# Kernel optimization log

Measured on AMD Instinct MI355X. Metric: run time of the kernel, lower is better.

Reference implementation:

```python
import jax, jax.numpy as jnp
import numpy as np

B, N, D = 4, 1024, 1024
T_ITER = 4
E_TYPES = 4  # edge_type_num; module loops over E_TYPES+1 with bitmask
ALPHA = 0.2


def _lin_w(key, out_f, in_f):
    # fan-avg uniform init from custom Linear
    bound = float(np.sqrt(3.0 / ((in_f + out_f) / 2.0)))
    return jax.random.uniform(key, (out_f, in_f), minval=-bound, maxval=bound, dtype=jnp.float32)


def setup_inputs() -> dict:
    key = jax.random.key(0)
    ks = jax.random.split(key, 32)
    inp = {}
    inp['ents'] = jax.random.normal(ks[0], (B, N, D), jnp.float32)
    inp['ent_mask'] = jnp.ones((B, N), jnp.float32)
    inp['q_encoding'] = jax.random.normal(ks[1], (B, D), jnp.float32)
    inp['adj'] = jax.random.randint(ks[2], (B, N, N), 0, E_TYPES + 1, dtype=jnp.int32)
    inp['types'] = 30  # bits 1..4 set -> edge types 1..4 active
    inp['init_mem'] = jax.random.normal(ks[3], (1, D), jnp.float32)
    inp['w_qin'] = _lin_w(ks[4], D, D); inp['b_qin'] = jnp.zeros((D,), jnp.float32)
    inp['w_qt'] = jnp.stack([_lin_w(ks[5 + t], D, D) for t in range(T_ITER)])
    inp['b_qt'] = jnp.zeros((T_ITER, D), jnp.float32)
    inp['w_pl'] = _lin_w(ks[9], D, D);  inp['b_pl'] = jnp.zeros((D,), jnp.float32)
    inp['w_pc'] = _lin_w(ks[10], D, D); inp['b_pc'] = jnp.zeros((D,), jnp.float32)
    inp['w_q'] = _lin_w(ks[11], D, 3 * D); inp['b_q'] = jnp.zeros((D,), jnp.float32)
    inp['w_k'] = _lin_w(ks[12], D, 3 * D); inp['b_k'] = jnp.zeros((D,), jnp.float32)
    inp['w_v'] = _lin_w(ks[13], D, 3 * D); inp['b_v'] = jnp.zeros((D,), jnp.float32)
    inp['w_pk'] = _lin_w(ks[14], D, D); inp['b_pk'] = jnp.zeros((D,), jnp.float32)
    inp['w_pv'] = _lin_w(ks[15], D, D); inp['b_pv'] = jnp.zeros((D,), jnp.float32)
    # wes: xavier_uniform(gain=1.414) on shape (2D, 1); stored flat as (E_TYPES, 2D)
    wb = 1.414 * float(np.sqrt(6.0 / (2 * D + 1)))
    inp['wes'] = jax.random.uniform(ks[16], (E_TYPES, 2 * D), minval=-wb, maxval=wb, dtype=jnp.float32)
    inp['w_mu'] = _lin_w(ks[17], D, 2 * D); inp['b_mu'] = jnp.zeros((D,), jnp.float32)
    inp['w_cb'] = _lin_w(ks[18], D, 2 * D); inp['b_cb'] = jnp.zeros((D,), jnp.float32)
    return inp


def _lin(x, w, b):
    return x @ w.T + b


def _qdgat_forward(ents, ent_mask, q_encoding, adj, types, init_mem,
                   w_qin, b_qin, w_qt, b_qt, w_pl, b_pl, w_pc, b_pc,
                   w_q, b_q, w_k, b_k, w_v, b_v, w_pk, b_pk, w_pv, b_pv,
                   wes, w_mu, b_mu, w_cb, b_cb):
    d = ents.shape[-1]
    x_loc = ents
    x_ctx = jnp.broadcast_to(init_mem, ents.shape)
    # eval mode: var-drop mask is ones scaled by ent_mask
    var_drop = ent_mask[:, :, None]
    adj_pos = adj > 0
    q_base = jax.nn.elu(_lin(q_encoding, w_qin, b_qin))
    n_types = wes.shape[0] + 1  # self.edge_type_num = edge_type_num + 1
    for t in range(T_ITER):
        cmd = _lin(q_base, w_qt[t], b_qt[t])                      # [B,D]
        xc = x_ctx * var_drop
        pl = _lin(x_loc, w_pl, b_pl)
        pc = _lin(xc, w_pc, b_pc)
        x_joint = jnp.concatenate([x_loc, xc, pl * pc], axis=-1)   # [B,N,3D]
        q = _lin(x_joint, w_q, b_q)                               # [B,N,D]
        k = _lin(x_joint, w_k, b_k) * _lin(cmd, w_pk, b_pk)[:, None, :]
        v = _lin(x_joint, w_v, b_v) * _lin(cmd, w_pv, b_pv)[:, None, :]
        # edge_score[b,i,j] = sum over active types T of (adj==T) * (q_i . we[:D] + k_j . we[D:])
        # equivalent to matmul((cat(q_i,k_j) * (adj==T)), we) without materializing [B,N,N,2D]
        edge_score = jnp.zeros(adj.shape, jnp.float32)
        for i in range(n_types):
            if (types >> i) & 1 == 1:
                w1, w2 = wes[i - 1, :d], wes[i - 1, d:]  # i=0 aliases wes[-1], as in torch
                s = (q @ w1)[:, :, None] + (k @ w2)[:, None, :]    # [B,N,N]
                edge_score = edge_score + jnp.where(adj == i, s, 0.0)
        e = jnp.where(edge_score > 0, edge_score, ALPHA * edge_score)  # leaky relu
        logits = jnp.where(adj_pos, e, jnp.float32(-9e15))
        prob = jax.nn.softmax(logits, axis=-1)                     # [B,N,N]
        message = jnp.einsum('bij,bjd->bid', prob, v)
        x_ctx = _lin(jnp.concatenate([xc, message], axis=-1), w_mu, b_mu)
    return _lin(jnp.concatenate([x_loc, x_ctx], axis=-1), w_cb, b_cb)


def reference(ents, ent_mask, q_encoding, adj, types, init_mem,
              w_qin, b_qin, w_qt, b_qt, w_pl, b_pl, w_pc, b_pc,
              w_q, b_q, w_k, b_k, w_v, b_v, w_pk, b_pk, w_pv, b_pv,
              wes, w_mu, b_mu, w_cb, b_cb):
    return _qdgat_forward(ents, ent_mask, q_encoding, adj, types, init_mem,
                          w_qin, b_qin, w_qt, b_qt, w_pl, b_pl, w_pc, b_pc,
                          w_q, b_q, w_k, b_k, w_v, b_v, w_pk, b_pk, w_pv, b_pv,
                          wes, w_mu, b_mu, w_cb, b_cb)
```

## Files before the change

### kernel.cpp

```cpp
#include <hip/hip_runtime.h>
#include <hip/hip_bf16.h>
#include <stdint.h>
#include <stddef.h>


typedef __hip_bfloat16 bf16;
typedef __attribute__((ext_vector_type(8))) short short8;
typedef __attribute__((ext_vector_type(4))) float floatx4;

#define NB 4
#define NN 1024
#define DD 1024
#define NT_ITER 4
#define MM (NB * NN)

static __device__ __forceinline__ float b2f(bf16 x) { return __bfloat162float(x); }
static __device__ __forceinline__ bf16 f2b(float x) { return __float2bfloat16(x); }
static __device__ __forceinline__ unsigned short f2bu(float x) {
    bf16 h = __float2bfloat16(x);
    unsigned short u;
    __builtin_memcpy(&u, &h, 2);
    return u;
}
static __device__ __forceinline__ float bu2f(unsigned short u) {
    unsigned int t = (unsigned int)u << 16;
    float f;
    __builtin_memcpy(&f, &t, 4);
    return f;
}

static __device__ __forceinline__ void gl_lds16(const void* g, void* l) {
    __builtin_amdgcn_global_load_lds(
        (const __attribute__((address_space(1))) unsigned int*)g,
        (__attribute__((address_space(3))) unsigned int*)l, 16, 0, 0);
}

template <int N>
static __device__ __forceinline__ void s_wait_vmcnt() {
    if constexpr (N == 0)      asm volatile("s_waitcnt vmcnt(0)" ::: "memory");
    else if constexpr (N == 4) asm volatile("s_waitcnt vmcnt(4)" ::: "memory");
    else if constexpr (N == 6) asm volatile("s_waitcnt vmcnt(6)" ::: "memory");
    else if constexpr (N == 8) asm volatile("s_waitcnt vmcnt(8)" ::: "memory");
}

__global__ void k_f2b(const float* __restrict__ src, bf16* __restrict__ dst, int n4) {
    int i = blockIdx.x * 256 + threadIdx.x;
    if (i >= n4) return;
    float4 v = ((const float4*)src)[i];
    ushort4 o;
    o.x = f2bu(v.x); o.y = f2bu(v.y); o.z = f2bu(v.z); o.w = f2bu(v.w);
    ((ushort4*)dst)[i] = o;
}

__global__ void k_transw(const float* __restrict__ src, bf16* __restrict__ dst) {
    __shared__ float tile[32][33];
    int c0 = blockIdx.x * 32;
    int r0 = blockIdx.y * 32;
    int tx = threadIdx.x, ty = threadIdx.y;
    for (int i = 0; i < 32; i += 8)
        tile[ty + i][tx] = src[(size_t)(r0 + ty + i) * 3072 + c0 + tx];
    __syncthreads();
    for (int i = 0; i < 32; i += 8)
        dst[(size_t)(c0 + ty + i) * 1024 + r0 + tx] = f2b(tile[tx][ty + i]);
}

__global__ void k_adjcode(const int* __restrict__ adj, const int* __restrict__ typesPtr,
                          unsigned char* __restrict__ code, int n4) {
    int i = blockIdx.x * 256 + threadIdx.x;
    if (i >= n4) return;
    int types = typesPtr[0];
    int4 a4 = ((const int4*)adj)[i];
    uchar4 c;
    int a;
    a = a4.x; c.x = (a == 0) ? 255 : (((types >> a) & 1) ? (unsigned char)(a - 1) : 254);
    a = a4.y; c.y = (a == 0) ? 255 : (((types >> a) & 1) ? (unsigned char)(a - 1) : 254);
    a = a4.z; c.z = (a == 0) ? 255 : (((types >> a) & 1) ? (unsigned char)(a - 1) : 254);
    a = a4.w; c.w = (a == 0) ? 255 : (((types >> a) & 1) ? (unsigned char)(a - 1) : 254);
    ((uchar4*)code)[i] = c;
}

__global__ void k_build_sc(const float* __restrict__ pk, const float* __restrict__ wes,
                           bf16* __restrict__ Aq, bf16* __restrict__ Ak) {
    int i = blockIdx.x * 256 + threadIdx.x;
    int half = i >> 16;
    int j = i & 65535;
    int row = j >> 10, d = j & 1023;
    if (half == 0) {
        Aq[j] = (row < 4) ? f2b(wes[(size_t)row * 2048 + d]) : f2b(0.f);
    } else {
        int t = row >> 4, b = (row >> 2) & 3, e = row & 3;
        Ak[j] = f2b(pk[((size_t)t * NB + b) * DD + d] * wes[(size_t)e * 2048 + 1024 + d]);
    }
}

__global__ __launch_bounds__(256) void k_qbase(const float* __restrict__ qenc, const float* __restrict__ w,
                                               const float* __restrict__ b, float* __restrict__ out) {
    int o = blockIdx.x * 4 + (threadIdx.x >> 6);
    int lane = threadIdx.x & 63;
    int n = o >> 2, r = o & 3;
    const float* xr = qenc + (size_t)r * DD;
    const float* wr = w + (size_t)n * DD;
    float s = 0.f;
    for (int d = lane; d < DD; d += 64) s += xr[d] * wr[d];
    for (int off = 32; off; off >>= 1) s += __shfl_down(s, off);
    if (lane == 0) {
        s += b[n];
        out[(size_t)r * DD + n] = s > 0.f ? s : (expf(s) - 1.0f);
    }
}

__global__ __launch_bounds__(256) void k_cmd(const float* __restrict__ qb, const float* __restrict__ w_qt,
                                             const float* __restrict__ b_qt, float* __restrict__ cmd) {
    int o = blockIdx.x * 4 + (threadIdx.x >> 6);
    int lane = threadIdx.x & 63;
    int r = o & 3, n = (o >> 2) & 1023, t = o >> 12;
    const float* xr = qb + (size_t)r * DD;
    const float* wr = w_qt + ((size_t)t * DD + n) * DD;
    float s = 0.f;
    for (int d = lane; d < DD; d += 64) s += xr[d] * wr[d];
    for (int off = 32; off; off >>= 1) s += __shfl_down(s, off);
    if (lane == 0) cmd[((size_t)t * NB + r) * DD + n] = s + b_qt[t * DD + n];
}

__global__ __launch_bounds__(256) void k_pkpv(const float* __restrict__ cmd,
                                              const float* __restrict__ w_pk, const float* __restrict__ b_pk,
                                              const float* __restrict__ w_pv, const float* __restrict__ b_pv,
                                              float* __restrict__ pk, float* __restrict__ pv) {
    int o = blockIdx.x * 4 + (threadIdx.x >> 6);
    int lane = threadIdx.x & 63;
    int n = o >> 5, half = (o >> 4) & 1, pair = o & 15;
    const float* xr = cmd + (size_t)pair * DD;
    const float* wr = (half ? w_pv : w_pk) + (size_t)n * DD;
    float s = 0.f;
    for (int d = lane; d < DD; d += 64) s += xr[d] * wr[d];
    for (int off = 32; off; off >>= 1) s += __shfl_down(s, off);
    if (lane == 0)
        (half ? pv : pk)[(size_t)pair * DD + n] = s + (half ? b_pv : b_pk)[n];
}

__global__ void k_consts(const float* __restrict__ b_q, const float* __restrict__ b_k,
                         const float* __restrict__ pk, const float* __restrict__ wes,
                         float* __restrict__ cq, float* __restrict__ ck) {
    int o = blockIdx.x;
    int lane = threadIdx.x;
    float s = 0.f;
    if (o < 4) {
        for (int d = lane; d < 1024; d += 64) s += b_q[d] * wes[(size_t)o * 2048 + d];
    } else {
        int oo = o - 4;
        int t = oo >> 4, b = (oo >> 2) & 3, e = oo & 3;
        for (int d = lane; d < 1024; d += 64)
            s += b_k[d] * pk[((size_t)t * NB + b) * DD + d] * wes[(size_t)e * 2048 + 1024 + d];
    }
    for (int off = 32; off; off >>= 1) s += __shfl_down(s, off);
    if (lane == 0) {
        if (o < 4) cq[o] = s;
        else ck[o - 4] = s;
    }
}

__global__ __launch_bounds__(256) void k_qakb2(const bf16* __restrict__ ents, const bf16* __restrict__ xc,
                                               const bf16* __restrict__ plpc,
                                               const float* __restrict__ wqtw, const float* __restrict__ wkeff_t,
                                               const float* __restrict__ cq, const float* __restrict__ ck_t,
                                               float* __restrict__ qa, float* __restrict__ kb) {
    __shared__ float red[4][8];
    int m = blockIdx.x;
    int b = m >> 10;
    int t = threadIdx.x;
    float aq[4] = {0.f, 0.f, 0.f, 0.f}, ak[4] = {0.f, 0.f, 0.f, 0.f};
    const bf16* rows[3] = {ents + (size_t)m * DD, xc + (size_t)m * DD, plpc + (size_t)m * DD};
#pragma unroll
    for (int c = 0; c < 3; ++c) {
        ushort4 rv = *(const ushort4*)(rows[c] + 4 * t);
        float xv0 = bu2f(rv.x), xv1 = bu2f(rv.y), xv2 = bu2f(rv.z), xv3 = bu2f(rv.w);
        const float* wq = wqtw + c * 1024 + 4 * t;
        const float* wk = wkeff_t + (size_t)b * 4 * 3072 + c * 1024 + 4 * t;
#pragma unroll
        for (int e = 0; e < 4; ++e) {
            float4 q4 = *(const float4*)(wq + (size_t)e * 3072);
            float4 k4 = *(const float4*)(wk + (size_t)e * 3072);
            aq[e] += xv0 * q4.x + xv1 * q4.y + xv2 * q4.z + xv3 * q4.w;
            ak[e] += xv0 * k4.x + xv1 * k4.y + xv2 * k4.z + xv3 * k4.w;
        }
    }
#pragma unroll
    for (int e = 0; e < 4; ++e) {
        float v = aq[e];
        for (int o = 32; o; o >>= 1) v += __shfl_down(v, o);
        if ((t & 63) == 0) red[t >> 6][e] = v;
        v = ak[e];
        for (int o = 32; o; o >>= 1) v += __shfl_down(v, o);
        if ((t & 63) == 0) red[t >> 6][e + 4] = v;
    }
    __syncthreads();
    if (t < 8) {
        float s = red[0][t] + red[1][t] + red[2][t] + red[3][t];
        if (t < 4) qa[(size_t)m * 4 + t] = s + cq[t];
        else kb[(size_t)m * 4 + (t - 4)] = s + ck_t[b * 4 + (t - 4)];
    }
}

__global__ void k_init(const bf16* __restrict__ initm_bf, const float* __restrict__ mask,
                       bf16* __restrict__ x_ctx, bf16* __restrict__ xc) {
    int i = blockIdx.x * 256 + threadIdx.x;
    uint4 v = ((const uint4*)initm_bf)[i & 127];
    ((uint4*)x_ctx)[i] = v;
    float mk = mask[i >> 7];
    unsigned short* u = (unsigned short*)&v;
#pragma unroll
    for (int j = 0; j < 8; ++j) u[j] = f2bu(bu2f(u[j]) * mk);
    ((uint4*)xc)[i] = v;
}

template <int WM, int WN>
__device__ __forceinline__ void gemm_core(
    const bf16* __restrict__ A0, const bf16* __restrict__ A1, const bf16* __restrict__ A2,
    const bf16* __restrict__ W, const float* __restrict__ bias, void* __restrict__ C,
    const void* __restrict__ mul, const float* __restrict__ addC, bf16* __restrict__ C2,
    int mulmode, int storef32, int nchunks, int ldw, int ldc,
    int bm, int bn) {
    constexpr int BM = WM * 2;
    constexpr int BN = WN * 2;
    constexpr int MI = WM / 16;
    constexpr int NI = WN / 16;
    constexpr int SEGS = (BM + BN) / 8;
    constexpr int SPW = SEGS / 4;
    __shared__ bf16 sAB[3][(BM + BN) * 64];

    const int t = threadIdx.x;
    const int lane = t & 63;
    const int w = t >> 6;
    const int wm = (w & 1) * WM, wn = (w >> 1) * WN;
    const int srow = lane >> 3;
    const int scol = ((lane & 7) * 8) ^ (srow << 3);

    floatx4 acc[MI][NI];
#pragma unroll
    for (int i = 0; i < MI; ++i)
#pragma unroll
        for (int j = 0; j < NI; ++j) acc[i][j] = (floatx4){0.f, 0.f, 0.f, 0.f};

    const int lrow = lane & 15;
    const int kq = (lane >> 4) * 8;
    const int kx = (lane & 7) << 3;
    const int ktiles = nchunks * 16;

    auto stage = [&](int buf, int kt) {
        const int cidx = kt >> 4;
        const bf16* Ac = (cidx == 0) ? A0 : (cidx == 1 ? A1 : A2);
        const int klocal = (kt & 15) * 64;
        const int kglob = kt * 64;
#pragma unroll
        for (int s = 0; s < SPW; ++s) {
            int c = w * SPW + s;
            if (c < BM / 8) {
                const bf16* src = Ac + ((size_t)(bm * BM + c * 8 + srow)) * 1024 + klocal + scol;
                gl_lds16(src, &sAB[buf][c * 512]);
            } else {
                const bf16* src = W + ((size_t)(bn * BN + (c - BM / 8) * 8 + srow)) * (size_t)ldw + kglob + scol;
                gl_lds16(src, &sAB[buf][c * 512]);
            }
        }
    };

    stage(0, 0);
    if (ktiles > 1) stage(1, 1);
    int cur = 0, sb = 2;
    for (int kt = 0; kt < ktiles; ++kt) {
        if (kt + 1 < ktiles) s_wait_vmcnt<SPW>();
        else s_wait_vmcnt<0>();
        __builtin_amdgcn_s_barrier();
        __builtin_amdgcn_sched_barrier(0);
        short8 af[2][MI], bfr[2][NI];
#pragma unroll
        for (int ks = 0; ks < 2; ++ks) {
            const int ko = (ks * 32 + kq) ^ kx;
#pragma unroll
            for (int mi = 0; mi < MI; ++mi)
                af[ks][mi] = *(const short8*)&sAB[cur][(wm + mi * 16 + lrow) * 64 + ko];
#pragma unroll
            for (int ni = 0; ni < NI; ++ni)
                bfr[ks][ni] = *(const short8*)&sAB[cur][BM * 64 + (wn + ni * 16 + lrow) * 64 + ko];
        }
        if (kt + 2 < ktiles) stage(sb, kt + 2);
        __builtin_amdgcn_s_setprio(1);
#pragma unroll
        for (int ks = 0; ks < 2; ++ks)
#pragma unroll
            for (int mi = 0; mi < MI; ++mi)
#pragma unroll
                for (int ni = 0; ni < NI; ++ni)
                    acc[mi][ni] = __builtin_amdgcn_mfma_f32_16x16x32_bf16(af[ks][mi], bfr[ks][ni], acc[mi][ni], 0, 0, 0);
        __builtin_amdgcn_s_setprio(0);
        asm volatile("s_waitcnt lgkmcnt(0)" ::: "memory");
        __builtin_amdgcn_sched_barrier(0);
        cur = (cur == 2) ? 0 : cur + 1;
        sb = (sb == 2) ? 0 : sb + 1;
    }

    const int qrow = (lane >> 4) * 4;
#pragma unroll
    for (int mi = 0; mi < MI; ++mi) {
#pragma unroll
        for (int ni = 0; ni < NI; ++ni) {
            int gn = bn * BN + wn + ni * 16 + lrow;
            float bv = bias ? bias[gn] : 0.f;
#pragma unroll
            for (int r = 0; r < 4; ++r) {
                int gm = bm * BM + wm + mi * 16 + qrow + r;
                size_t ci = (size_t)gm * (size_t)ldc + gn;
                float val = acc[mi][ni][r] + bv;
                if (addC) val += addC[ci];
                if (mulmode == 1)
                    val *= b2f(((const bf16*)mul)[(size_t)gm * 1024 + gn]);
                else if (mulmode == 2)
                    val *= ((const float*)mul)[(size_t)(gm >> 10) * 1024 + gn];
                if (storef32) {
                    ((float*)C)[ci] = val;
                } else {
                    ((bf16*)C)[ci] = f2b(val);
                    if (mulmode == 3)
                        C2[ci] = f2b(val * ((const float*)mul)[gm]);
                }
            }
        }
    }
}

template <int WM, int WN>
__global__ __launch_bounds__(256) void k_gemm_t(
    const bf16* __restrict__ A0, const bf16* __restrict__ A1, const bf16* __restrict__ A2,
    const bf16* __restrict__ W, const float* __restrict__ bias, void* __restrict__ C,
    const void* __restrict__ mul, const float* __restrict__ addC, bf16* __restrict__ C2,
    int mulmode, int storef32, int nchunks, int ldw, int ldc,
    long long sA, long long sW, long long sC) {
    int bz = blockIdx.z;
    const bf16* A0b = A0 + (size_t)bz * sA;
    const bf16* Wb = W + (size_t)bz * sW;
    void* Cb = storef32 ? (void*)((float*)C + (size_t)bz * sC)
                        : (void*)((bf16*)C + (size_t)bz * sC);
    gemm_core<WM, WN>(A0b, A1, A2, Wb, bias, Cb, mul, addC, C2, mulmode, storef32, nchunks, ldw, ldc,
                      blockIdx.x, blockIdx.y);
}

__global__ void k_transpose(const bf16* __restrict__ v, bf16* __restrict__ vT) {
    __shared__ bf16 tile[32][33];
    int b = blockIdx.z;
    int n0 = blockIdx.x * 32, d0 = blockIdx.y * 32;
    int tx = threadIdx.x, ty = threadIdx.y;
    for (int i = 0; i < 32; i += 8)
        tile[ty + i][tx] = v[((size_t)b * NN + n0 + ty + i) * DD + d0 + tx];
    __syncthreads();
    for (int i = 0; i < 32; i += 8)
        vT[((size_t)b * DD + d0 + ty + i) * NN + n0 + tx] = tile[tx][ty + i];
}

__global__ __launch_bounds__(256) void k_attn(const unsigned char* __restrict__ code,
                                              const float* __restrict__ qa,
                                              const float* __restrict__ kb,
                                              bf16* __restrict__ prob) {
    __shared__ float red[4];
    __shared__ float red2[4];
    int m = blockIdx.x;
    int b = m >> 10;
    int t = threadIdx.x;
    float qa0 = qa[(size_t)m * 4 + 0];
    float qa1 = qa[(size_t)m * 4 + 1];
    float qa2 = qa[(size_t)m * 4 + 2];
    float qa3 = qa[(size_t)m * 4 + 3];
    const float* kbb = kb + (size_t)(b << 10) * 4;

    uchar4 c4 = *(const uchar4*)(code + (size_t)m * NN + 4 * t);
    float l0, l1, l2, l3;
    {
        unsigned char cc[4] = {c4.x, c4.y, c4.z, c4.w};
        float lv[4];
#pragma unroll
        for (int jj = 0; jj < 4; ++jj) {
            int j = 4 * t + jj;
            float4 k4 = *(const float4*)(kbb + (size_t)j * 4);
            unsigned char c = cc[jj];
            float kv = (c == 0) ? k4.x : ((c == 1) ? k4.y : ((c == 2) ? k4.z : k4.w));
            float qv = (c == 0) ? qa0 : ((c == 1) ? qa1 : ((c == 2) ? qa2 : qa3));
            float s = qv + kv;
            s = s > 0.f ? s : 0.2f * s;
            lv[jj] = (c == 255) ? -9.0e15f : ((c == 254) ? 0.f : s);
        }
        l0 = lv[0]; l1 = lv[1]; l2 = lv[2]; l3 = lv[3];
    }

    float lmax = fmaxf(fmaxf(l0, l1), fmaxf(l2, l3));
    for (int o = 32; o > 0; o >>= 1) lmax = fmaxf(lmax, __shfl_down(lmax, o));
    if ((t & 63) == 0) red[t >> 6] = lmax;
    __syncthreads();
    lmax = fmaxf(fmaxf(red[0], red[1]), fmaxf(red[2], red[3]));

    float e0 = __expf(l0 - lmax), e1 = __expf(l1 - lmax);
    float e2 = __expf(l2 - lmax), e3 = __expf(l3 - lmax);
    float lsum = (e0 + e1) + (e2 + e3);
    for (int o = 32; o > 0; o >>= 1) lsum += __shfl_down(lsum, o);
    if ((t & 63) == 0) red2[t >> 6] = lsum;
    __syncthreads();
    lsum = red2[0] + red2[1] + red2[2] + red2[3];
    float inv = 1.0f / lsum;

    ushort4 o4;
    o4.x = f2bu(e0 * inv); o4.y = f2bu(e1 * inv);
    o4.z = f2bu(e2 * inv); o4.w = f2bu(e3 * inv);
    ((ushort4*)(prob + (size_t)m * NN))[t] = o4;
}

extern "C" void kernel_launch(void* const* d_in, const int* in_sizes, int n_in,
                              void* d_out, int out_size, void* d_ws, size_t ws_size,
                              hipStream_t stream) {
    const float* ents = (const float*)d_in[0];
    const float* mask = (const float*)d_in[1];
    const float* qenc = (const float*)d_in[2];
    const int* adj = (const int*)d_in[3];
    const int* types = (const int*)d_in[4];
    const float* initm = (const float*)d_in[5];
    const float* w_qin = (const float*)d_in[6];
    const float* b_qin = (const float*)d_in[7];
    const float* w_qt = (const float*)d_in[8];
    const float* b_qt = (const float*)d_in[9];
    const float* w_pl = (const float*)d_in[10];
    const float* b_pl = (const float*)d_in[11];
    const float* w_pc = (const float*)d_in[12];
    const float* b_pc = (const float*)d_in[13];
    const float* w_q = (const float*)d_in[14];
    const float* b_q = (const float*)d_in[15];
    const float* w_k = (const float*)d_in[16];
    const float* b_k = (const float*)d_in[17];
    const float* w_v = (const float*)d_in[18];
    const float* b_v = (const float*)d_in[19];
    const float* w_pk = (const float*)d_in[20];
    const float* b_pk = (const float*)d_in[21];
    const float* w_pv = (const float*)d_in[22];
    const float* b_pv = (const float*)d_in[23];
    const float* wes = (const float*)d_in[24];
    const float* w_mu = (const float*)d_in[25];
    const float* b_mu = (const float*)d_in[26];
    const float* w_cb = (const float*)d_in[27];
    const float* b_cb = (const float*)d_in[28];
    (void)in_sizes; (void)n_in; (void)out_size; (void)ws_size;

    char* p = (char*)d_ws;
    auto carve = [&](size_t bytes) {
        char* r = p;
        p += (bytes + 255) & ~(size_t)255;
        return r;
    };
    float* q_base = (float*)carve((size_t)NB * DD * 4);
    float* cmd = (float*)carve((size_t)NT_ITER * NB * DD * 4);
    float* pk = (float*)carve((size_t)NT_ITER * NB * DD * 4);
    float* pv = (float*)carve((size_t)NT_ITER * NB * DD * 4);
    float* qa = (float*)carve((size_t)MM * 4 * 4);
    float* kb = (float*)carve((size_t)MM * 4 * 4);
    float* wqtw = (float*)carve((size_t)64 * 3072 * 4);
    float* wkeff = (float*)carve((size_t)64 * 3072 * 4);
    float* cq = (float*)carve(4 * 4);
    float* ck = (float*)carve(64 * 4);
    float* vent = (float*)carve((size_t)MM * DD * 4);
    bf16* initm_bf = (bf16*)carve((size_t)DD * 2);
    bf16* ents_bf = (bf16*)carve((size_t)MM * DD * 2);
    bf16* wpl_bf = (bf16*)carve((size_t)DD * DD * 2);
    bf16* wpc_bf = (bf16*)carve((size_t)DD * DD * 2);
    bf16* wv_bf = (bf16*)carve((size_t)DD * 3 * DD * 2);
    bf16* wmu_bf = (bf16*)carve((size_t)DD * 2 * DD * 2);
    bf16* wcb_bf = (bf16*)carve((size_t)DD * 2 * DD * 2);
    bf16* wqT_bf = (bf16*)carve((size_t)3 * DD * DD * 2);
    bf16* wkT_bf = (bf16*)carve((size_t)3 * DD * DD * 2);
    bf16* Aq = (bf16*)carve((size_t)64 * DD * 2);
    bf16* Ak = (bf16*)carve((size_t)64 * DD * 2);
    unsigned char* code = (unsigned char*)carve((size_t)MM * NN);
    bf16* x_ctx = (bf16*)carve((size_t)MM * DD * 2);
    bf16* xc = (bf16*)carve((size_t)MM * DD * 2);
    bf16* pl = (bf16*)carve((size_t)MM * DD * 2);
    bf16* plpc = (bf16*)carve((size_t)MM * DD * 2);
    bf16* vbuf = (bf16*)carve((size_t)MM * DD * 2);
    bf16* msg = (bf16*)carve((size_t)MM * DD * 2);
    bf16* prob = (bf16*)carve((size_t)NB * NN * NN * 2);
    bf16* vT = plpc;

    const dim3 blk(256);
    const dim3 g128(32, 16, 1);
    const dim3 gMsg(8, 16, NB);
    const dim3 gPre(1, 48, 1);

    k_f2b<<<1, blk, 0, stream>>>(initm, initm_bf, DD / 4);
    k_f2b<<<4096, blk, 0, stream>>>(ents, ents_bf, MM * DD / 4);
    k_f2b<<<1024, blk, 0, stream>>>(w_pl, wpl_bf, DD * DD / 4);
    k_f2b<<<1024, blk, 0, stream>>>(w_pc, wpc_bf, DD * DD / 4);
    k_f2b<<<3072, blk, 0, stream>>>(w_v, wv_bf, DD * 3 * DD / 4);
    k_f2b<<<2048, blk, 0, stream>>>(w_mu, wmu_bf, DD * 2 * DD / 4);
    k_f2b<<<2048, blk, 0, stream>>>(w_cb, wcb_bf, DD * 2 * DD / 4);
    k_transw<<<dim3(96, 32), dim3(32, 8), 0, stream>>>(w_q, wqT_bf);
    k_transw<<<dim3(96, 32), dim3(32, 8), 0, stream>>>(w_k, wkT_bf);
    k_adjcode<<<4096, blk, 0, stream>>>(adj, types, code, MM * NN / 4);

    k_qbase<<<1024, blk, 0, stream>>>(qenc, w_qin, b_qin, q_base);
    k_cmd<<<4096, blk, 0, stream>>>(q_base, w_qt, b_qt, cmd);
    k_pkpv<<<8192, blk, 0, stream>>>(cmd, w_pk, b_pk, w_pv, b_pv, pk, pv);
    k_init<<<2048, blk, 0, stream>>>(initm_bf, mask, x_ctx, xc);

    k_build_sc<<<512, blk, 0, stream>>>(pk, wes, Aq, Ak);
    k_consts<<<68, 64, 0, stream>>>(b_q, b_k, pk, wes, cq, ck);
    k_gemm_t<32, 32><<<gPre, blk, 0, stream>>>(Aq, nullptr, nullptr, wqT_bf, nullptr, wqtw,
                                               nullptr, nullptr, nullptr, 0, 1, 1, 1024, 3072, 0, 0, 0);
    k_gemm_t<32, 32><<<gPre, blk, 0, stream>>>(Ak, nullptr, nullptr, wkT_bf, nullptr, wkeff,
                                               nullptr, nullptr, nullptr, 0, 1, 1, 1024, 3072, 0, 0, 0);

    k_gemm_t<64, 32><<<g128, blk, 0, stream>>>(ents_bf, nullptr, nullptr, wpl_bf, b_pl, pl,
                                               nullptr, nullptr, nullptr, 0, 0, 1, 1024, 1024, 0, 0, 0);
    k_gemm_t<64, 32><<<g128, blk, 0, stream>>>(ents_bf, nullptr, nullptr, wv_bf, nullptr, vent,
                                               nullptr, nullptr, nullptr, 0, 1, 1, 3072, 1024, 0, 0, 0);

    for (int t = 0; t < NT_ITER; ++t) {
        k_gemm_t<64, 32><<<g128, blk, 0, stream>>>(xc, nullptr, nullptr, wpc_bf, b_pc, plpc,
                                                   pl, nullptr, nullptr, 1, 0, 1, 1024, 1024, 0, 0, 0);
        k_gemm_t<64, 32><<<g128, blk, 0, stream>>>(xc, plpc, nullptr, wv_bf + 1024, b_v, vbuf,
                                                   pv + (size_t)t * NB * DD, vent, nullptr, 2, 0, 2, 3072, 1024, 0, 0, 0);
        k_qakb2<<<4096, blk, 0, stream>>>(ents_bf, xc, plpc,
                                          wqtw, wkeff + (size_t)t * 16 * 3072,
                                          cq, ck + t * 16, qa, kb);
        k_transpose<<<dim3(32, 32, NB), dim3(32, 8), 0, stream>>>(vbuf, vT);
        k_attn<<<4096, blk, 0, stream>>>(code, qa, kb, prob);
        k_gemm_t<64, 32><<<gMsg, blk, 0, stream>>>(prob, nullptr, nullptr, vT, nullptr, msg,
                                                   nullptr, nullptr, nullptr, 0, 0, 1, 1024, 1024,
                                                   (long long)NN * NN, (long long)DD * NN, (long long)NN * DD);
        k_gemm_t<64, 32><<<g128, blk, 0, stream>>>(xc, msg, nullptr, wmu_bf, b_mu, x_ctx,
                                                   mask, nullptr, xc, 3, 0, 2, 2048, 1024, 0, 0, 0);
    }
    k_gemm_t<64, 32><<<g128, blk, 0, stream>>>(ents_bf, x_ctx, nullptr, wcb_bf, b_cb, (float*)d_out,
                                               nullptr, nullptr, nullptr, 0, 1, 2, 2048, 1024, 0, 0, 0);
}
```

Before: 940.5 us.

## Fuse per-iteration xc GEMMs into one wide GEMM and batch conversion launches

All three GEMMs that read xc (w_pc, the xc slice of w_v, the xc slice of w_mu) become one wider GEMM over a concatenated weight matrix built once at setup. A new epilogue mode routes each output column segment to its own destination, writing fp32 partial sums that the later v and mu GEMMs add back while doing only the remaining K=1024 half. The startup fp32->bf16 conversions and the two weight transposes are each merged into a single launch. This cuts launches and repeated xc reads and gives a larger grid, at the cost of extra fp32 intermediate buffers that must be written and read again.

After: 1.074 ms. 14.2% more time.

```diff
diff --git a/kernel.cpp b/kernel.cpp
--- a/kernel.cpp
+++ b/kernel.cpp
@@ -43,17 +43,38 @@
     else if constexpr (N == 8) asm volatile("s_waitcnt vmcnt(8)" ::: "memory");
 }
 
-__global__ void k_f2b(const float* __restrict__ src, bf16* __restrict__ dst, int n4) {
-    int i = blockIdx.x * 256 + threadIdx.x;
-    if (i >= n4) return;
-    float4 v = ((const float4*)src)[i];
+__global__ void k_f2b_all(const float* __restrict__ initm, const float* __restrict__ ents,
+                          const float* __restrict__ wpl, const float* __restrict__ wpc,
+                          const float* __restrict__ wv, const float* __restrict__ wmu,
+                          const float* __restrict__ wcb,
+                          bf16* __restrict__ initm_bf, bf16* __restrict__ ents_bf,
+                          bf16* __restrict__ wpl_bf, bf16* __restrict__ wpc_bf,
+                          bf16* __restrict__ wv_bf, bf16* __restrict__ wmu_bf,
+                          bf16* __restrict__ wcb_bf) {
+    long i = (long)blockIdx.x * 256 + threadIdx.x;
+    const float* src;
+    bf16* dst;
+    long off;
+    if (i < 1048832) {
+        if (i < 256) { src = initm; dst = initm_bf; off = i; }
+        else { src = ents; dst = ents_bf; off = i - 256; }
+    } else if (i < 1573120) {
+        if (i < 1310976) { src = wpl; dst = wpl_bf; off = i - 1048832; }
+        else { src = wpc; dst = wpc_bf; off = i - 1310976; }
+    } else if (i < 2359552) { src = wv; dst = wv_bf; off = i - 1573120; }
+    else if (i < 2883840) { src = wmu; dst = wmu_bf; off = i - 2359552; }
+    else { src = wcb; dst = wcb_bf; off = i - 2883840; }
+    float4 v = ((const float4*)src)[off];
     ushort4 o;
     o.x = f2bu(v.x); o.y = f2bu(v.y); o.z = f2bu(v.z); o.w = f2bu(v.w);
-    ((ushort4*)dst)[i] = o;
-}
-
-__global__ void k_transw(const float* __restrict__ src, bf16* __restrict__ dst) {
+    ((ushort4*)dst)[off] = o;
+}
+
+__global__ void k_transw2(const float* __restrict__ srcq, const float* __restrict__ srck,
+                          bf16* __restrict__ dstq, bf16* __restrict__ dstk) {
     __shared__ float tile[32][33];
+    const float* src = blockIdx.z ? srck : srcq;
+    bf16* dst = blockIdx.z ? dstk : dstq;
     int c0 = blockIdx.x * 32;
     int r0 = blockIdx.y * 32;
     int tx = threadIdx.x, ty = threadIdx.y;
@@ -62,6 +83,25 @@
     __syncthreads();
     for (int i = 0; i < 32; i += 8)
         dst[(size_t)(c0 + ty + i) * 1024 + r0 + tx] = f2b(tile[tx][ty + i]);
+}
+
+__global__ void k_buildcomb(const bf16* __restrict__ wpc_bf, const bf16* __restrict__ wv_bf,
+                            const bf16* __restrict__ wmu_bf,
+                            const float* __restrict__ b_pc, const float* __restrict__ b_v,
+                            const float* __restrict__ b_mu,
+                            bf16* __restrict__ wcomb, float* __restrict__ bcomb) {
+    int i = blockIdx.x * 256 + threadIdx.x;
+    if (i < 786432) {
+        int r = i >> 8;
+        int c4 = (i & 255) * 4;
+        ushort4 v;
+        if (r < 1024)      v = *(const ushort4*)(wpc_bf + (size_t)r * 1024 + c4);
+        else if (r < 2048) v = *(const ushort4*)(wv_bf + (size_t)(r - 1024) * 3072 + 1024 + c4);
+        else               v = *(const ushort4*)(wmu_bf + (size_t)(r - 2048) * 2048 + c4);
+        ((ushort4*)wcomb)[i] = v;
+    }
+    if (i < 3072)
+        bcomb[i] = (i < 1024) ? b_pc[i] : (i < 2048 ? b_v[i - 1024] : b_mu[i - 2048]);
 }
 
 __global__ void k_adjcode(const int* __restrict__ adj, const int* __restrict__ typesPtr,
@@ -218,6 +258,7 @@
     const bf16* __restrict__ A0, const bf16* __restrict__ A1, const bf16* __restrict__ A2,
     const bf16* __restrict__ W, const float* __restrict__ bias, void* __restrict__ C,
     const void* __restrict__ mul, const float* __restrict__ addC, bf16* __restrict__ C2,
+    float* __restrict__ X1, float* __restrict__ X2,
     int mulmode, int storef32, int nchunks, int ldw, int ldc,
     int bm, int bn) {
     constexpr int BM = WM * 2;
@@ -309,19 +350,30 @@
 #pragma unroll
             for (int r = 0; r < 4; ++r) {
                 int gm = bm * BM + wm + mi * 16 + qrow + r;
-                size_t ci = (size_t)gm * (size_t)ldc + gn;
                 float val = acc[mi][ni][r] + bv;
-                if (addC) val += addC[ci];
-                if (mulmode == 1)
-                    val *= b2f(((const bf16*)mul)[(size_t)gm * 1024 + gn]);
-                else if (mulmode == 2)
-                    val *= ((const float*)mul)[(size_t)(gm >> 10) * 1024 + gn];
-                if (storef32) {
-                    ((float*)C)[ci] = val;
+                if (mulmode == 4) {
+                    int seg = gn >> 10, gl = gn & 1023;
+                    size_t li = (size_t)gm * 1024 + gl;
+                    if (seg == 0)
+                        ((bf16*)C)[li] = f2b(val * b2f(((const bf16*)mul)[li]));
+                    else if (seg == 1)
+                        X1[li] = val + addC[li];
+                    else
+                        X2[li] = val;
                 } else {
-                    ((bf16*)C)[ci] = f2b(val);
-                    if (mulmode == 3)
-                        C2[ci] = f2b(val * ((const float*)mul)[gm]);
+                    size_t ci = (size_t)gm * (size_t)ldc + gn;
+                    if (addC) val += addC[ci];
+                    if (mulmode == 1)
+                        val *= b2f(((const bf16*)mul)[(size_t)gm * 1024 + gn]);
+                    else if (mulmode == 2)
+                        val *= ((const float*)mul)[(size_t)(gm >> 10) * 1024 + gn];
+                    if (storef32) {
+                        ((float*)C)[ci] = val;
+                    } else {
+                        ((bf16*)C)[ci] = f2b(val);
+                        if (mulmode == 3)
+                            C2[ci] = f2b(val * ((const float*)mul)[gm]);
+                    }
                 }
             }
         }
@@ -333,6 +385,7 @@
     const bf16* __restrict__ A0, const bf16* __restrict__ A1, const bf16* __restrict__ A2,
     const bf16* __restrict__ W, const float* __restrict__ bias, void* __restrict__ C,
     const void* __restrict__ mul, const float* __restrict__ addC, bf16* __restrict__ C2,
+    float* __restrict__ X1, float* __restrict__ X2,
     int mulmode, int storef32, int nchunks, int ldw, int ldc,
     long long sA, long long sW, long long sC) {
     int bz = blockIdx.z;
@@ -340,7 +393,8 @@
     const bf16* Wb = W + (size_t)bz * sW;
     void* Cb = storef32 ? (void*)((float*)C + (size_t)bz * sC)
                         : (void*)((bf16*)C + (size_t)bz * sC);
-    gemm_core<WM, WN>(A0b, A1, A2, Wb, bias, Cb, mul, addC, C2, mulmode, storef32, nchunks, ldw, ldc,
+    gemm_core<WM, WN>(A0b, A1, A2, Wb, bias, Cb, mul, addC, C2, X1, X2,
+                      mulmode, storef32, nchunks, ldw, ldc,
                       blockIdx.x, blockIdx.y);
 }
 
@@ -461,7 +515,10 @@
     float* wkeff = (float*)carve((size_t)64 * 3072 * 4);
     float* cq = (float*)carve(4 * 4);
     float* ck = (float*)carve(64 * 4);
+    float* bcomb = (float*)carve((size_t)3072 * 4);
     float* vent = (float*)carve((size_t)MM * DD * 4);
+    float* vxc = (float*)carve((size_t)MM * DD * 4);
+    float* muxc = (float*)carve((size_t)MM * DD * 4);
     bf16* initm_bf = (bf16*)carve((size_t)DD * 2);
     bf16* ents_bf = (bf16*)carve((size_t)MM * DD * 2);
     bf16* wpl_bf = (bf16*)carve((size_t)DD * DD * 2);
@@ -471,6 +528,7 @@
     bf16* wcb_bf = (bf16*)carve((size_t)DD * 2 * DD * 2);
     bf16* wqT_bf = (bf16*)carve((size_t)3 * DD * DD * 2);
     bf16* wkT_bf = (bf16*)carve((size_t)3 * DD * DD * 2);
+    bf16* wcomb = (bf16*)carve((size_t)3 * DD * DD * 2);
     bf16* Aq = (bf16*)carve((size_t)64 * DD * 2);
     bf16* Ak = (bf16*)carve((size_t)64 * DD * 2);
     unsigned char* code = (unsigned char*)carve((size_t)MM * NN);
@@ -485,19 +543,15 @@
 
     const dim3 blk(256);
     const dim3 g128(32, 16, 1);
+    const dim3 gBig(32, 48, 1);
     const dim3 gMsg(8, 16, NB);
     const dim3 gPre(1, 48, 1);
 
-    k_f2b<<<1, blk, 0, stream>>>(initm, initm_bf, DD / 4);
-    k_f2b<<<4096, blk, 0, stream>>>(ents, ents_bf, MM * DD / 4);
-    k_f2b<<<1024, blk, 0, stream>>>(w_pl, wpl_bf, DD * DD / 4);
-    k_f2b<<<1024, blk, 0, stream>>>(w_pc, wpc_bf, DD * DD / 4);
-    k_f2b<<<3072, blk, 0, stream>>>(w_v, wv_bf, DD * 3 * DD / 4);
-    k_f2b<<<2048, blk, 0, stream>>>(w_mu, wmu_bf, DD * 2 * DD / 4);
-    k_f2b<<<2048, blk, 0, stream>>>(w_cb, wcb_bf, DD * 2 * DD / 4);
-    k_transw<<<dim3(96, 32), dim3(32, 8), 0, stream>>>(w_q, wqT_bf);
-    k_transw<<<dim3(96, 32), dim3(32, 8), 0, stream>>>(w_k, wkT_bf);
+    k_f2b_all<<<13313, blk, 0, stream>>>(initm, ents, w_pl, w_pc, w_v, w_mu, w_cb,
+                                         initm_bf, ents_bf, wpl_bf, wpc_bf, wv_bf, wmu_bf, wcb_bf);
+    k_transw2<<<dim3(96, 32, 2), dim3(32, 8), 0, stream>>>(w_q, w_k, wqT_bf, wkT_bf);
     k_adjcode<<<4096, blk, 0, stream>>>(adj, types, code, MM * NN / 4);
+    k_buildcomb<<<3072, blk, 0, stream>>>(wpc_bf, wv_bf, wmu_bf, b_pc, b_v, b_mu, wcomb, bcomb);
 
     k_qbase<<<1024, blk, 0, stream>>>(qenc, w_qin, b_qin, q_base);
     k_cmd<<<4096, blk, 0, stream>>>(q_base, w_qt, b_qt, cmd);
@@ -507,31 +561,40 @@
     k_build_sc<<<512, blk, 0, stream>>>(pk, wes, Aq, Ak);
     k_consts<<<68, 64, 0, stream>>>(b_q, b_k, pk, wes, cq, ck);
     k_gemm_t<32, 32><<<gPre, blk, 0, stream>>>(Aq, nullptr, nullptr, wqT_bf, nullptr, wqtw,
-                                               nullptr, nullptr, nullptr, 0, 1, 1, 1024, 3072, 0, 0, 0);
+                                               nullptr, nullptr, nullptr, nullptr, nullptr,
+                                               0, 1, 1, 1024, 3072, 0, 0, 0);
     k_gemm_t<32, 32><<<gPre, blk, 0, stream>>>(Ak, nullptr, nullptr, wkT_bf, nullptr, wkeff,
-                                               nullptr, nullptr, nullptr, 0, 1, 1, 1024, 3072, 0, 0, 0);
+                                               nullptr, nullptr, nullptr, nullptr, nullptr,
+                                               0, 1, 1, 1024, 3072, 0, 0, 0);
 
     k_gemm_t<64, 32><<<g128, blk, 0, stream>>>(ents_bf, nullptr, nullptr, wpl_bf, b_pl, pl,
-                                               nullptr, nullptr, nullptr, 0, 0, 1, 1024, 1024, 0, 0, 0);
+                                               nullptr, nullptr, nullptr, nullptr, nullptr,
+                                               0, 0, 1, 1024, 1024, 0, 0, 0);
     k_gemm_t<64, 32><<<g128, blk, 0, stream>>>(ents_bf, nullptr, nullptr, wv_bf, nullptr, vent,
-                                               nullptr, nullptr, nullptr, 0, 1, 1, 3072, 1024, 0, 0, 0);
+                                               nullptr, nullptr, nullptr, nullptr, nullptr,
+                                               0, 1, 1, 3072, 1024, 0, 0, 0);
 
     for (int t = 0; t < NT_ITER; ++t) {
-        k_gemm_t<64, 32><<<g128, blk, 0, stream>>>(xc, nullptr, nullptr, wpc_bf, b_pc, plpc,
-                                                   pl, nullptr, nullptr, 1, 0, 1, 1024, 1024, 0, 0, 0);
-        k_gemm_t<64, 32><<<g128, blk, 0, stream>>>(xc, plpc, nullptr, wv_bf + 1024, b_v, vbuf,
-                                                   pv + (size_t)t * NB * DD, vent, nullptr, 2, 0, 2, 3072, 1024, 0, 0, 0);
+        k_gemm_t<64, 32><<<gBig, blk, 0, stream>>>(xc, nullptr, nullptr, wcomb, bcomb, plpc,
+                                                   pl, vent, nullptr, vxc, muxc,
+                                                   4, 0, 1, 1024, 1024, 0, 0, 0);
+        k_gemm_t<64, 32><<<g128, blk, 0, stream>>>(plpc, nullptr, nullptr, wv_bf + 2048, nullptr, vbuf,
+                                                   pv + (size_t)t * NB * DD, vxc, nullptr, nullptr, nullptr,
+                                                   2, 0, 1, 3072, 1024, 0, 0, 0);
         k_qakb2<<<4096, blk, 0, stream>>>(ents_bf, xc, plpc,
                                           wqtw, wkeff + (size_t)t * 16 * 3072,
                                           cq, ck + t * 16, qa, kb);
         k_transpose<<<dim3(32, 32, NB), dim3(32, 8), 0, stream>>>(vbuf, vT);
         k_attn<<<4096, blk, 0, stream>>>(code, qa, kb, prob);
         k_gemm_t<64, 32><<<gMsg, blk, 0, stream>>>(prob, nullptr, nullptr, vT, nullptr, msg,
-                                                   nullptr, nullptr, nullptr, 0, 0, 1, 1024, 1024,
+                                                   nullptr, nullptr, nullptr, nullptr, nullptr,
+                                                   0, 0, 1, 1024, 1024,
                                                    (long long)NN * NN, (long long)DD * NN, (long long)NN * DD);
-        k_gemm_t<64, 32><<<g128, blk, 0, stream>>>(xc, msg, nullptr, wmu_bf, b_mu, x_ctx,
-                                                   mask, nullptr, xc, 3, 0, 2, 2048, 1024, 0, 0, 0);
+        k_gemm_t<64, 32><<<g128, blk, 0, stream>>>(msg, nullptr, nullptr, wmu_bf + 1024, nullptr, x_ctx,
+                                                   mask, muxc, xc, nullptr, nullptr,
+                                                   3, 0, 1, 2048, 1024, 0, 0, 0);
     }
     k_gemm_t<64, 32><<<g128, blk, 0, stream>>>(ents_bf, x_ctx, nullptr, wcb_bf, b_cb, (float*)d_out,
-                                               nullptr, nullptr, nullptr, 0, 1, 2, 2048, 1024, 0, 0, 0);
-}
+                                               nullptr, nullptr, nullptr, nullptr, nullptr,
+                                               0, 1, 2, 2048, 1024, 0, 0, 0);
+}
```
